# Performance work log

Measured on AMD Instinct MI355X. Metric: run time of the kernel, lower is better.

The kernel has to match this reference:

```python
import jax, jax.numpy as jnp
import numpy as np

NUM_HEADS = 16


def setup_inputs() -> dict:
    key = jax.random.key(0)
    ks = jax.random.split(key, 5)
    B, S, D = 2, 2048, 1024
    scale = 0.02
    return {
        "x": jax.random.normal(ks[0], (B, S, D), dtype=jnp.float32),
        "Wq": jax.random.normal(ks[1], (D, D), dtype=jnp.float32) * scale,
        "Wk": jax.random.normal(ks[2], (D, D), dtype=jnp.float32) * scale,
        "Wv": jax.random.normal(ks[3], (D, D), dtype=jnp.float32) * scale,
        "Wo": jax.random.normal(ks[4], (D, D), dtype=jnp.float32) * scale,
        "bo": jnp.zeros((D,), dtype=jnp.float32),
    }


def reference(x, Wq, Wk, Wv, Wo, bo):
    B, S, D = x.shape
    H = NUM_HEADS
    Dh = D // H
    # project and split heads -> [B, H, S, Dh]
    q = (x @ Wq).reshape(B, S, H, Dh).transpose(0, 2, 1, 3)
    k = (x @ Wk).reshape(B, S, H, Dh).transpose(0, 2, 1, 3)
    v = (x @ Wv).reshape(B, S, H, Dh).transpose(0, 2, 1, 3)
    # full causal attention scores [B, H, S, S]
    scores = jnp.einsum("bhqd,bhkd->bhqk", q, k)
    causal_mask = jnp.triu(jnp.ones((S, S), dtype=bool), k=1)
    scores = jnp.where(causal_mask, -jnp.inf, scores)
    attn = jax.nn.softmax(scores / jnp.sqrt(jnp.float32(Dh)), axis=-1)
    ctx = jnp.einsum("bhqk,bhkd->bhqd", attn, v)
    ctx = ctx.transpose(0, 2, 1, 3).reshape(B, S, D)
    return ctx @ Wo + bo
```

## Files before the change

kernel.cpp:

```cpp
#include <hip/hip_runtime.h>
#include <hip/hip_bf16.h>
#include <math.h>

typedef __bf16 bf16_t;
typedef bf16_t bf16x4 __attribute__((ext_vector_type(4)));
typedef bf16_t bf16x8 __attribute__((ext_vector_type(8)));
typedef float f32x4 __attribute__((ext_vector_type(4)));

#define MFMA16(a, b, c) __builtin_amdgcn_mfma_f32_16x16x32_bf16(a, b, c, 0, 0, 0)
#define NEG_BIG (-1e30f)
#define QSCALE 0.18033688f

#define GLL16(gp, lp)                                                          \
    __builtin_amdgcn_global_load_lds(                                          \
        (const __attribute__((address_space(1))) unsigned int*)(gp),           \
        (__attribute__((address_space(3))) unsigned int*)(lp), 16, 0, 0)


__global__ __launch_bounds__(256) void prep(const float* __restrict__ x,
                                            const float* __restrict__ Wq,
                                            const float* __restrict__ Wk,
                                            const float* __restrict__ Wv,
                                            const float* __restrict__ Wo,
                                            bf16_t* __restrict__ Xb,
                                            bf16_t* __restrict__ WTqkv,
                                            bf16_t* __restrict__ WoT) {
    __shared__ float tile[32][33];
    const int z = blockIdx.z;
    const int tx = threadIdx.x, ty = threadIdx.y;
    if (z == 4) {
        int i0 = (((blockIdx.y * 32 + blockIdx.x) * 256) + ty * 32 + tx) * 4;
        for (int j = 0; j < 4; j++) {
            int i = i0 + j * 1048576;
            float4 v = *(const float4*)(x + i);
            Xb[i + 0] = (bf16_t)v.x;
            Xb[i + 1] = (bf16_t)v.y;
            Xb[i + 2] = (bf16_t)v.z;
            Xb[i + 3] = (bf16_t)v.w;
        }
    } else {
        const float* W = (z == 0) ? Wq : (z == 1) ? Wk : (z == 2) ? Wv : Wo;
        bf16_t* WT = (z < 3) ? (WTqkv + (size_t)z * 1048576) : WoT;
        int bx = blockIdx.x * 32, by = blockIdx.y * 32;
        for (int i = 0; i < 32; i += 8)
            tile[ty + i][tx] = W[(size_t)(by + ty + i) * 1024 + bx + tx];
        __syncthreads();
        for (int i = 0; i < 32; i += 8)
            WT[(size_t)(bx + ty + i) * 1024 + by + tx] = (bf16_t)tile[tx][ty + i];
    }
}

__global__ __launch_bounds__(256) void gemm_qkv(const bf16_t* __restrict__ X,
                                                const bf16_t* __restrict__ WT,
                                                bf16_t* __restrict__ Qd,
                                                bf16_t* __restrict__ Kd,
                                                bf16_t* __restrict__ Vd) {
    __shared__ bf16_t AsmF[2 * 64 * 64];
    __shared__ bf16_t BsmF[2 * 128 * 64];
    const int which = blockIdx.z;
    const bf16_t* Wt = WT + (size_t)which * 1048576;
    const int bm = blockIdx.y * 64;
    const int bn = blockIdx.x * 128;
    const int tid = threadIdx.x;
    const int wave = tid >> 6, lane = tid & 63;
    const int wm = (wave >> 1) * 32, wn = (wave & 1) * 64;
    const int col = lane & 15, quad = lane >> 4;
    const int cswz = col & 7;
    const int lr8 = lane >> 3;
    const int jg = (lane & 7) ^ lr8;

    const int arow = wave * 16 + lr8;
    const int brow = wave * 32 + lr8;
    const bf16_t* gA = X  + (size_t)(bm + arow) * 1024 + jg * 8;
    const bf16_t* gB = Wt + (size_t)(bn + brow) * 1024 + jg * 8;

    auto stage = [&](int k0, int bsel) {
        bf16_t* lA = AsmF + bsel * 4096 + wave * 1024;
        bf16_t* lB = BsmF + bsel * 8192 + wave * 2048;
        for (int j = 0; j < 2; j++)
            GLL16(gA + (size_t)j * 8192 + k0, lA + j * 512);
        for (int j = 0; j < 4; j++)
            GLL16(gB + (size_t)j * 8192 + k0, lB + j * 512);
    };

    f32x4 acc[2][4] = {};

    stage(0, 0);
    for (int kt = 0; kt < 16; kt++) {
        __syncthreads();
        if (kt + 1 < 16) stage((kt + 1) * 64, (kt + 1) & 1);

        const bf16_t* Abuf = AsmF + (kt & 1) * 4096;
        const bf16_t* Bbuf = BsmF + (kt & 1) * 8192;
        for (int ks = 0; ks < 2; ks++) {
            bf16x8 af[2], bfr[4];
            for (int mi = 0; mi < 2; mi++)
                af[mi] = *(const bf16x8*)&Abuf[(wm + mi * 16 + col) * 64 +
                                               (((ks << 2) + quad) ^ cswz) * 8];
            for (int ni = 0; ni < 4; ni++)
                bfr[ni] = *(const bf16x8*)&Bbuf[(wn + ni * 16 + col) * 64 +
                                                (((ks << 2) + quad) ^ cswz) * 8];
            if (which != 2) {
                for (int mi = 0; mi < 2; mi++)
                    for (int ni = 0; ni < 4; ni++)
                        acc[mi][ni] = MFMA16(af[mi], bfr[ni], acc[mi][ni]);
            } else {
                for (int mi = 0; mi < 2; mi++)
                    for (int ni = 0; ni < 4; ni++)
                        acc[mi][ni] = MFMA16(bfr[ni], af[mi], acc[mi][ni]);
            }
        }
    }

    if (which != 2) {
        const float sc = (which == 0) ? QSCALE : 1.0f;
        for (int mi = 0; mi < 2; mi++) {
            for (int ni = 0; ni < 4; ni++) {
                int mbase = bm + wm + mi * 16 + quad * 4;
                int n = bn + wn + ni * 16 + col;
                int h = n >> 6, dh = n & 63;
                for (int r = 0; r < 4; r++) {
                    int m = mbase + r;
                    int b = m >> 11, s = m & 2047;
                    size_t bh = (size_t)b * 16 + h;
                    bf16_t val = (bf16_t)(acc[mi][ni][r] * sc);
                    if (which == 0) Qd[(bh * 2048 + s) * 64 + dh] = val;
                    else            Kd[(bh * 2048 + s) * 64 + dh] = val;
                }
            }
        }
    } else {
        for (int mi = 0; mi < 2; mi++) {
            for (int ni = 0; ni < 4; ni++) {
                int nbase = bn + wn + ni * 16 + quad * 4;
                int m = bm + wm + mi * 16 + col;
                int b = m >> 11, s = m & 2047;
                for (int r = 0; r < 4; r++) {
                    int n = nbase + r;
                    int h = n >> 6, dh = n & 63;
                    size_t bh = (size_t)b * 16 + h;
                    Vd[(bh * 64 + dh) * 2048 + s] = (bf16_t)acc[mi][ni][r];
                }
            }
        }
    }
}

#define PSD 72
__global__ __launch_bounds__(256) void attn(const bf16_t* __restrict__ Q,
                                            const bf16_t* __restrict__ K,
                                            const bf16_t* __restrict__ VT,
                                            bf16_t* __restrict__ CTX) {
    __shared__ bf16_t KsF[2 * 64 * 64];
    __shared__ bf16_t VsF[2 * 64 * 64];
    __shared__ bf16_t Ps[4][16][PSD];

    const int bidx = blockIdx.x;
    const int bh = bidx & 31;
    const int qt = 31 - (bidx >> 5);
    const int tid = threadIdx.x;
    const int wave = tid >> 6, lane = tid & 63;
    const int col = lane & 15, quad = lane >> 4;
    const int cswz = col & 7;
    const int lr8 = lane >> 3;
    const int jg = (lane & 7) ^ lr8;

    const bf16_t* Qb = Q + (size_t)bh * 2048 * 64;
    const bf16_t* Kb = K + (size_t)bh * 2048 * 64;
    const bf16_t* Vb = VT + (size_t)bh * 64 * 2048;

    const int strow = wave * 16 + lr8;
    const bf16_t* gK = Kb + (size_t)strow * 64 + jg * 8;
    const bf16_t* gV = Vb + (size_t)strow * 2048 + jg * 8;

    const int b_ = bh >> 4, h_ = bh & 15;

    bf16x8 ones;
    for (int i = 0; i < 8; i++) ones[i] = (bf16_t)1.0f;

    auto stage = [&](int k0, int bsel) {
        bf16_t* lK = KsF + bsel * 4096 + wave * 1024;
        bf16_t* lV = VsF + bsel * 4096 + wave * 1024;
        for (int j = 0; j < 2; j++) {
            GLL16(gK + (size_t)(k0 + j * 8) * 64, lK + j * 512);
            GLL16(gV + (size_t)(k0 + j * 8 * 2048), lV + j * 512);
        }
    };

    stage(0, 0);

    const int q0 = qt * 64;
    const int qrow = q0 + wave * 16 + col;
    const bf16x8 qf0 = *(const bf16x8*)&Qb[(size_t)qrow * 64 + quad * 8];
    const bf16x8 qf1 = *(const bf16x8*)&Qb[(size_t)qrow * 64 + 32 + quad * 8];

    f32x4 o[4] = {};
    f32x4 accl = {};

    const int nt = qt + 1;
    for (int g = 0; g < nt; g++) {
        __syncthreads();
        if (g + 1 < nt) stage((g + 1) * 64, (g + 1) & 1);

        const int bsel = g & 1;
        const bf16_t* Kbuf = KsF + bsel * 4096;
        const bf16_t* Vbuf = VsF + bsel * 4096;
        const bool diag = (g == qt);

        for (int ksub = 0; ksub < 4; ksub++) {
            bf16x8 a0 = *(const bf16x8*)&Kbuf[(ksub * 16 + col) * 64 +
                                              (quad ^ cswz) * 8];
            bf16x8 a1 = *(const bf16x8*)&Kbuf[(ksub * 16 + col) * 64 +
                                              ((4 + quad) ^ cswz) * 8];
            f32x4 z = {};
            z = MFMA16(a0, qf0, z);
            z = MFMA16(a1, qf1, z);
            if (diag) {
                for (int r = 0; r < 4; r++) {
                    int lk = ksub * 16 + quad * 4 + r;
                    if (lk > wave * 16 + col) z[r] = NEG_BIG;
                }
            }
            bf16x4 pw;
            for (int r = 0; r < 4; r++)
                pw[r] = (bf16_t)exp2f(z[r]);
            *(bf16x4*)&Ps[wave][col][ksub * 16 + quad * 4] = pw;
        }

        for (int ck = 0; ck < 2; ck++) {
            bf16x8 pf = *(const bf16x8*)&Ps[wave][col][ck * 32 + quad * 8];
            accl = MFMA16(pf, ones, accl);
            for (int d = 0; d < 4; d++) {
                bf16x8 vf = *(const bf16x8*)&Vbuf[(d * 16 + col) * 64 +
                                                  (((ck << 2) + quad) ^ cswz) * 8];
                o[d] = MFMA16(pf, vf, o[d]);
            }
        }
    }

    for (int d = 0; d < 4; d++) {
        for (int r = 0; r < 4; r++) {
            int s = q0 + wave * 16 + quad * 4 + r;
            CTX[((size_t)(b_ * 2048 + s)) * 1024 + h_ * 64 + d * 16 + col] =
                (bf16_t)(o[d][r] / fmaxf(accl[r], 1e-20f));
        }
    }
}

__global__ __launch_bounds__(256) void gemm_out(const bf16_t* __restrict__ X,
                                                const bf16_t* __restrict__ WT,
                                                const float* __restrict__ BO,
                                                float* __restrict__ OUT) {
    __shared__ bf16_t AsmF[2 * 64 * 64];
    __shared__ bf16_t BsmF[2 * 128 * 64];
    const int bm = blockIdx.y * 64;
    const int bn = blockIdx.x * 128;
    const int tid = threadIdx.x;
    const int wave = tid >> 6, lane = tid & 63;
    const int wm = (wave >> 1) * 32, wn = (wave & 1) * 64;
    const int col = lane & 15, quad = lane >> 4;
    const int cswz = col & 7;
    const int lr8 = lane >> 3;
    const int jg = (lane & 7) ^ lr8;

    const int arow = wave * 16 + lr8;
    const int brow = wave * 32 + lr8;
    const bf16_t* gA = X  + (size_t)(bm + arow) * 1024 + jg * 8;
    const bf16_t* gB = WT + (size_t)(bn + brow) * 1024 + jg * 8;

    auto stage = [&](int k0, int bsel) {
        bf16_t* lA = AsmF + bsel * 4096 + wave * 1024;
        bf16_t* lB = BsmF + bsel * 8192 + wave * 2048;
        for (int j = 0; j < 2; j++)
            GLL16(gA + (size_t)j * 8192 + k0, lA + j * 512);
        for (int j = 0; j < 4; j++)
            GLL16(gB + (size_t)j * 8192 + k0, lB + j * 512);
    };

    f32x4 acc[2][4] = {};

    stage(0, 0);
    for (int kt = 0; kt < 16; kt++) {
        __syncthreads();
        if (kt + 1 < 16) stage((kt + 1) * 64, (kt + 1) & 1);

        const bf16_t* Abuf = AsmF + (kt & 1) * 4096;
        const bf16_t* Bbuf = BsmF + (kt & 1) * 8192;
        for (int ks = 0; ks < 2; ks++) {
            bf16x8 af[2], bfr[4];
            for (int mi = 0; mi < 2; mi++)
                af[mi] = *(const bf16x8*)&Abuf[(wm + mi * 16 + col) * 64 +
                                               (((ks << 2) + quad) ^ cswz) * 8];
            for (int ni = 0; ni < 4; ni++)
                bfr[ni] = *(const bf16x8*)&Bbuf[(wn + ni * 16 + col) * 64 +
                                                (((ks << 2) + quad) ^ cswz) * 8];
            for (int mi = 0; mi < 2; mi++)
                for (int ni = 0; ni < 4; ni++)
                    acc[mi][ni] = MFMA16(af[mi], bfr[ni], acc[mi][ni]);
        }
    }

    for (int mi = 0; mi < 2; mi++) {
        for (int ni = 0; ni < 4; ni++) {
            int mbase = bm + wm + mi * 16 + quad * 4;
            int n = bn + wn + ni * 16 + col;
            float bov = BO[n];
            for (int r = 0; r < 4; r++) {
                int m = mbase + r;
                OUT[(size_t)m * 1024 + n] = acc[mi][ni][r] + bov;
            }
        }
    }
}

extern "C" void kernel_launch(void* const* d_in, const int* in_sizes, int n_in,
                              void* d_out, int out_size, void* d_ws, size_t ws_size,
                              hipStream_t stream) {
    const float* x  = (const float*)d_in[0];
    const float* Wq = (const float*)d_in[1];
    const float* Wk = (const float*)d_in[2];
    const float* Wv = (const float*)d_in[3];
    const float* Wo = (const float*)d_in[4];
    const float* bo = (const float*)d_in[5];
    float* out = (float*)d_out;

    const size_t MEG = 1048576;
    bf16_t* base  = (bf16_t*)d_ws;
    bf16_t* Xb    = base;
    bf16_t* WTqkv = base + 4 * MEG;
    bf16_t* WoT   = base + 7 * MEG;
    bf16_t* Qb    = base + 8 * MEG;
    bf16_t* Kb    = base + 12 * MEG;
    bf16_t* Vb    = base + 16 * MEG;
    bf16_t* Cb    = base + 20 * MEG;

    prep<<<dim3(32, 32, 5), dim3(32, 8), 0, stream>>>(x, Wq, Wk, Wv, Wo,
                                                      Xb, WTqkv, WoT);
    gemm_qkv<<<dim3(8, 64, 3), 256, 0, stream>>>(Xb, WTqkv, Qb, Kb, Vb);
    attn<<<1024, 256, 0, stream>>>(Qb, Kb, Vb, Cb);
    gemm_out<<<dim3(8, 64), 256, 0, stream>>>(Cb, WoT, bo, out);
}
```

Baseline: 180.8 us.

## Use 128-row query tiles with 8 waves per attention block

The attention kernel now launches 512 blocks of 512 threads. Each block covers 128 query rows with 8 waves, so every staged 64-key K/V tile is shared by twice as many query rows, which halves global K/V traffic per query. The P scratch buffer changes from padded rows to an XOR-swizzled layout to avoid LDS bank conflicts. The first four waves skip the final diagonal tile. The cost is fewer blocks, more threads per block, and some idle waves on edge tiles.

Measured after the change: 187.1 us. 3.5% more time.

```diff
diff --git a/kernel.cpp b/kernel.cpp
--- a/kernel.cpp
+++ b/kernel.cpp
@@ -146,18 +146,17 @@
     }
 }
 
-#define PSD 72
-__global__ __launch_bounds__(256) void attn(const bf16_t* __restrict__ Q,
+__global__ __launch_bounds__(512) void attn(const bf16_t* __restrict__ Q,
                                             const bf16_t* __restrict__ K,
                                             const bf16_t* __restrict__ VT,
                                             bf16_t* __restrict__ CTX) {
     __shared__ bf16_t KsF[2 * 64 * 64];
     __shared__ bf16_t VsF[2 * 64 * 64];
-    __shared__ bf16_t Ps[4][16][PSD];
+    __shared__ bf16_t PsF[8 * 16 * 64];
 
     const int bidx = blockIdx.x;
     const int bh = bidx & 31;
-    const int qt = 31 - (bidx >> 5);
+    const int qi = 15 - (bidx >> 5);
     const int tid = threadIdx.x;
     const int wave = tid >> 6, lane = tid & 63;
     const int col = lane & 15, quad = lane >> 4;
@@ -169,7 +168,7 @@
     const bf16_t* Kb = K + (size_t)bh * 2048 * 64;
     const bf16_t* Vb = VT + (size_t)bh * 64 * 2048;
 
-    const int strow = wave * 16 + lr8;
+    const int strow = wave * 8 + lr8;
     const bf16_t* gK = Kb + (size_t)strow * 64 + jg * 8;
     const bf16_t* gV = Vb + (size_t)strow * 2048 + jg * 8;
 
@@ -178,62 +177,64 @@
     bf16x8 ones;
     for (int i = 0; i < 8; i++) ones[i] = (bf16_t)1.0f;
 
+    bf16_t* PsRow = PsF + wave * 1024 + col * 64;
+
     auto stage = [&](int k0, int bsel) {
-        bf16_t* lK = KsF + bsel * 4096 + wave * 1024;
-        bf16_t* lV = VsF + bsel * 4096 + wave * 1024;
-        for (int j = 0; j < 2; j++) {
-            GLL16(gK + (size_t)(k0 + j * 8) * 64, lK + j * 512);
-            GLL16(gV + (size_t)(k0 + j * 8 * 2048), lV + j * 512);
-        }
+        GLL16(gK + (size_t)k0 * 64, KsF + bsel * 4096 + wave * 512);
+        GLL16(gV + k0,              VsF + bsel * 4096 + wave * 512);
     };
 
     stage(0, 0);
 
-    const int q0 = qt * 64;
-    const int qrow = q0 + wave * 16 + col;
-    const bf16x8 qf0 = *(const bf16x8*)&Qb[(size_t)qrow * 64 + quad * 8];
-    const bf16x8 qf1 = *(const bf16x8*)&Qb[(size_t)qrow * 64 + 32 + quad * 8];
+    const int q0 = qi * 128;
+    const int qg = q0 + wave * 16 + col;
+    const bf16x8 qf0 = *(const bf16x8*)&Qb[(size_t)qg * 64 + quad * 8];
+    const bf16x8 qf1 = *(const bf16x8*)&Qb[(size_t)qg * 64 + 32 + quad * 8];
 
     f32x4 o[4] = {};
     f32x4 accl = {};
 
-    const int nt = qt + 1;
+    const int nt = 2 * qi + 2;
     for (int g = 0; g < nt; g++) {
         __syncthreads();
         if (g + 1 < nt) stage((g + 1) * 64, (g + 1) & 1);
 
-        const int bsel = g & 1;
-        const bf16_t* Kbuf = KsF + bsel * 4096;
-        const bf16_t* Vbuf = VsF + bsel * 4096;
-        const bool diag = (g == qt);
-
-        for (int ksub = 0; ksub < 4; ksub++) {
-            bf16x8 a0 = *(const bf16x8*)&Kbuf[(ksub * 16 + col) * 64 +
-                                              (quad ^ cswz) * 8];
-            bf16x8 a1 = *(const bf16x8*)&Kbuf[(ksub * 16 + col) * 64 +
-                                              ((4 + quad) ^ cswz) * 8];
-            f32x4 z = {};
-            z = MFMA16(a0, qf0, z);
-            z = MFMA16(a1, qf1, z);
-            if (diag) {
-                for (int r = 0; r < 4; r++) {
-                    int lk = ksub * 16 + quad * 4 + r;
-                    if (lk > wave * 16 + col) z[r] = NEG_BIG;
+        if (!(g == nt - 1 && wave < 4)) {
+            const int bsel = g & 1;
+            const bf16_t* Kbuf = KsF + bsel * 4096;
+            const bf16_t* Vbuf = VsF + bsel * 4096;
+            const bool edge = (g >= 2 * qi);
+            const int k0 = g * 64;
+
+            for (int ksub = 0; ksub < 4; ksub++) {
+                bf16x8 a0 = *(const bf16x8*)&Kbuf[(ksub * 16 + col) * 64 +
+                                                  (quad ^ cswz) * 8];
+                bf16x8 a1 = *(const bf16x8*)&Kbuf[(ksub * 16 + col) * 64 +
+                                                  ((4 + quad) ^ cswz) * 8];
+                f32x4 z = {};
+                z = MFMA16(a0, qf0, z);
+                z = MFMA16(a1, qf1, z);
+                if (edge) {
+                    for (int r = 0; r < 4; r++) {
+                        int key = k0 + ksub * 16 + quad * 4 + r;
+                        if (key > qg) z[r] = NEG_BIG;
+                    }
                 }
-            }
-            bf16x4 pw;
-            for (int r = 0; r < 4; r++)
-                pw[r] = (bf16_t)exp2f(z[r]);
-            *(bf16x4*)&Ps[wave][col][ksub * 16 + quad * 4] = pw;
-        }
-
-        for (int ck = 0; ck < 2; ck++) {
-            bf16x8 pf = *(const bf16x8*)&Ps[wave][col][ck * 32 + quad * 8];
-            accl = MFMA16(pf, ones, accl);
-            for (int d = 0; d < 4; d++) {
-                bf16x8 vf = *(const bf16x8*)&Vbuf[(d * 16 + col) * 64 +
-                                                  (((ck << 2) + quad) ^ cswz) * 8];
-                o[d] = MFMA16(pf, vf, o[d]);
+                bf16x4 pw;
+                for (int r = 0; r < 4; r++)
+                    pw[r] = (bf16_t)exp2f(z[r]);
+                *(bf16x4*)&PsRow[((ksub * 2 + (quad >> 1)) ^ cswz) * 8 +
+                                 (quad & 1) * 4] = pw;
+            }
+
+            for (int ck = 0; ck < 2; ck++) {
+                bf16x8 pf = *(const bf16x8*)&PsRow[((ck * 4 + quad) ^ cswz) * 8];
+                accl = MFMA16(pf, ones, accl);
+                for (int d = 0; d < 4; d++) {
+                    bf16x8 vf = *(const bf16x8*)&Vbuf[(d * 16 + col) * 64 +
+                                                      (((ck << 2) + quad) ^ cswz) * 8];
+                    o[d] = MFMA16(pf, vf, o[d]);
+                }
             }
         }
     }
@@ -337,6 +338,6 @@
     prep<<<dim3(32, 32, 5), dim3(32, 8), 0, stream>>>(x, Wq, Wk, Wv, Wo,
                                                       Xb, WTqkv, WoT);
     gemm_qkv<<<dim3(8, 64, 3), 256, 0, stream>>>(Xb, WTqkv, Qb, Kb, Vb);
-    attn<<<1024, 256, 0, stream>>>(Qb, Kb, Vb, Cb);
+    attn<<<512, 512, 0, stream>>>(Qb, Kb, Vb, Cb);
     gemm_out<<<dim3(8, 64), 256, 0, stream>>>(Cb, WoT, bo, out);
 }
```
